# Optimization experiments

Measured on AMD Instinct MI355X. Metric: run time of the kernel, lower is better.

Reference implementation:

```python
import jax, jax.numpy as jnp
import numpy as np

I_SIZE = 4096
H_SIZE = 2048
WIN = 10          # window_size
MAX_DEPTH = 6
EPS = 1e-9


def setup_inputs() -> dict:
    key = jax.random.key(0)
    ks = jax.random.split(key, 10)
    u = lambda k, s: jax.random.uniform(k, s, dtype=jnp.float32)
    n = lambda k, s: jax.random.normal(k, s, dtype=jnp.float32) * 0.02
    return {
        "input": u(ks[0], (WIN, I_SIZE)),
        "stack": u(ks[1], (1, H_SIZE, I_SIZE)),
        "stack_pointer": u(ks[2], (1, H_SIZE)),
        "input_pointer": u(ks[3], (1, WIN + 1)),
        "ff_w": n(ks[4], (I_SIZE, I_SIZE)), "ff_b": jnp.zeros((I_SIZE,), jnp.float32),
        "gate_w": n(ks[5], (2, 1)), "gate_b": jnp.zeros((2,), jnp.float32),
        "kin_w": n(ks[6], (I_SIZE, 2 * I_SIZE)), "kin_b": jnp.zeros((I_SIZE,), jnp.float32),
        "kouth_w": n(ks[7], (I_SIZE, I_SIZE)), "kouth_b": jnp.zeros((I_SIZE,), jnp.float32),
        "kouti_w": n(ks[8], (I_SIZE, I_SIZE)), "kouti_b": jnp.zeros((I_SIZE,), jnp.float32),
    }


def _forward(input, stack, stack_pointer, input_pointer,
             ff_w, ff_b, gate_w, gate_b, kin_w, kin_b,
             kouth_w, kouth_b, kouti_w, kouti_b):
    lsm = jax.nn.log_softmax
    lin = lambda x, w, b: jnp.matmul(x, w.T) + b

    def push(vec, stk, ptr):
        # stk: [1,H,I], ptr: [1,H], vec: [1,I] or [1,1,I]
        stk = stk * (1.0 - ptr)[..., None] + jnp.matmul(ptr[..., None], vec)
        ptr_new = jnp.concatenate([jnp.zeros((ptr.shape[0], 1), ptr.dtype), ptr[:, :-1]], axis=-1)
        return stk, ptr_new

    def pop(stk, ptr):
        ptr_new = jnp.concatenate([ptr[:, 1:], jnp.zeros((ptr.shape[0], 1), ptr.dtype)], axis=-1)
        s = jnp.sum(ptr_new, -1)                      # [1]
        norm = jnp.where(s > 0, ptr_new / jnp.where(s > 0, s, 1.0), ptr_new)
        outvec = jnp.matmul(norm, stk)                # [1,1,I]
        stk_new = (1.0 - ptr_new)[..., None] * stk
        ptr_new = ptr_new.at[:, 0].add(ptr[:, 0])
        return outvec, stk_new, ptr_new

    def get(inp, ptr):
        outvec = jnp.matmul(ptr[:, :-1], inp)         # [1,I]
        ptr_new = jnp.concatenate([jnp.zeros((ptr.shape[0], 1), ptr.dtype), ptr[:, :-1]], axis=-1)
        ptr_new = ptr_new.at[:, -1].add(ptr[:, -1])
        return outvec, ptr_new

    def kld(p, q):
        p = p + EPS
        q = q + EPS
        p = p / jnp.sum(p)
        q = q / jnp.sum(q)
        return jnp.sum(p * jnp.log(p / q))

    def calforward(invec, hvec):
        predvec = lsm(lin(hvec, ff_w, ff_b))
        perp_pred = kld(predvec, invec)
        inp_cat = jnp.concatenate([invec.reshape(1, 1, -1), hvec.reshape(1, 1, -1)], axis=-1)
        new_inp = jnp.exp(lsm(lin(inp_cat, kin_w, kin_b)))      # softmax, [1,1,I]
        proj_hvec = jnp.exp(lsm(lin(new_inp, kouth_w, kouth_b)))
        proj_invec = jnp.exp(lsm(lin(new_inp, kouti_w, kouti_b)))
        perp = perp_pred + kld(proj_invec, invec) / 2 + kld(proj_hvec, hvec) / 2
        gate = jnp.exp(lsm(lin(perp_pred.reshape(1), gate_w, gate_b)))  # [2]
        gate = jnp.where(jnp.sum(hvec) == 0, jnp.array([1.0, 0.0], gate.dtype),
                         jnp.where(jnp.sum(invec) == 0, jnp.array([0.0, 1.0], gate.dtype), gate))
        return gate, perp, new_inp

    stackmem, sptrmem, iptrmem, wldl, perps = [], [], [], [], []
    for ii in range(MAX_DEPTH):
        if ii == 0:
            invec, st1, sp1 = pop(stack, stack_pointer)
            hvec, st1, sp1 = pop(st1, sp1)
            gate, perp, new_inp = calforward(invec, hvec)
            st1, sp1 = push(new_inp, st1, sp1)
            stackmem.append(st1); sptrmem.append(sp1); iptrmem.append(input_pointer)
            wldl.append(gate[1]); perps.append(perp)
        else:
            ip2, st2, sp2 = input_pointer, stack, stack_pointer
            for _ in range(ii - 1):
                invec, ip2 = get(input, ip2)
                st2, sp2 = push(invec, st2, sp2)
            invec, ip2 = get(input, ip2)
            hvec, st2, sp2 = pop(st2, sp2)
            gate, perp, new_inp = calforward(invec, hvec)
            st2, sp2 = push(new_inp, st2, sp2)
            stackmem.append(st2); sptrmem.append(sp2); iptrmem.append(ip2)
            input_avail = 1.0 - ip2[0, -1]
            wldl.append((1.0 - wldl[ii - 1]) * gate[1] * input_avail)
            perps.append(perp)

    w = jnp.stack(wldl)
    w = w / jnp.sum(w)
    resperp = jnp.sum(w * jnp.stack(perps))
    new_stack = sum(w[i] * stackmem[i] for i in range(MAX_DEPTH))
    new_sp = sum(w[i] * sptrmem[i] for i in range(MAX_DEPTH))
    new_ip = sum(w[i] * iptrmem[i] for i in range(MAX_DEPTH))
    ssum = jnp.sum(new_sp, -1, keepdims=True)
    new_sp = jnp.where(ssum > 0, new_sp / jnp.where(ssum > 0, ssum, 1.0), new_sp)
    isum = jnp.sum(new_ip, -1, keepdims=True)
    new_ip = jnp.where(isum > 0, new_ip / jnp.where(isum > 0, isum, 1.0), new_ip)
    return resperp, new_stack, new_sp, new_ip


def reference(input, stack, stack_pointer, input_pointer,
              ff_w, ff_b, gate_w, gate_b, kin_w, kin_b,
              kouth_w, kouth_b, kouti_w, kouti_b):
    return _forward(input, stack, stack_pointer, input_pointer,
                    ff_w, ff_b, gate_w, gate_b, kin_w, kin_b,
                    kouth_w, kouth_b, kouti_w, kouti_b)
```

## Files before the change

kernel.cpp:

```cpp
#include <hip/hip_runtime.h>
#include <cfloat>
#include <cmath>

#define HH   2048
#define ISZ  4096
#define WN   10
#define ND   6
#define EPSF 1e-9f

#define O_WROW   0
#define O_GETW   14336
#define O_POPC   14464
#define O_AVAIL  14496
#define O_SCAL   14528
#define O_IPTR   14592
#define O_DFIN   14720
#define O_CNEW   27008
#define O_CFIN   39296
#define O_SPTR   88448
#define O_NEWINP 100736
#define O_G      125312
#define O_HVEC   145792
#define O_IVEC   170368
#define O_YFF    194944
#define O_Z1     219520
#define O_Z2     244096
#define O_YH     268672
#define O_YI     293248
#define O_RPART  317824

__device__ __forceinline__ float blockReduceSum(float v, float* sm){
  int ln = threadIdx.x & 63, w = threadIdx.x >> 6;
  #pragma unroll
  for (int o=32;o>0;o>>=1) v += __shfl_down(v,o);
  if (ln==0) sm[w]=v;
  __syncthreads();
  if (threadIdx.x==0){
    float r=0.f; int nw=(int)(blockDim.x>>6);
    for (int i=0;i<nw;i++) r+=sm[i];
    sm[16]=r;
  }
  __syncthreads();
  float r = sm[16];
  __syncthreads();
  return r;
}

template<int N>
__device__ __forceinline__ void bRedSumN(float* v, float* sm){
  int ln=threadIdx.x&63, w=threadIdx.x>>6;
  #pragma unroll
  for (int o=32;o>0;o>>=1){
    #pragma unroll
    for (int i=0;i<N;i++) v[i]+=__shfl_down(v[i],o);
  }
  if (ln==0){ for (int i=0;i<N;i++) sm[w*N+i]=v[i]; }
  __syncthreads();
  if (threadIdx.x==0){
    for (int i=0;i<N;i++){ float r=0.f; for (int q=0;q<16;q++) r+=sm[q*N+i]; sm[16*N+i]=r; }
  }
  __syncthreads();
  for (int i=0;i<N;i++) v[i]=sm[16*N+i];
  __syncthreads();
}

template<int N>
__device__ __forceinline__ void bRedMaxN(float* v, float* sm){
  int ln=threadIdx.x&63, w=threadIdx.x>>6;
  #pragma unroll
  for (int o=32;o>0;o>>=1){
    #pragma unroll
    for (int i=0;i<N;i++) v[i]=fmaxf(v[i],__shfl_down(v[i],o));
  }
  if (ln==0){ for (int i=0;i<N;i++) sm[w*N+i]=v[i]; }
  __syncthreads();
  if (threadIdx.x==0){
    for (int i=0;i<N;i++){ float r=-FLT_MAX; for (int q=0;q<16;q++) r=fmaxf(r,sm[q*N+i]); sm[16*N+i]=r; }
  }
  __syncthreads();
  for (int i=0;i<N;i++) v[i]=sm[16*N+i];
  __syncthreads();
}

__global__ __launch_bounds__(1024) void k_ptr_prep(
    const float* __restrict__ sp0g, const float* __restrict__ ip0g,
    float* __restrict__ ws)
{
  __shared__ float sp[HH], q[HH], D[HH];
  __shared__ float c[4][HH];
  __shared__ float red[17];
  const int d   = blockIdx.x;
  const int tid = threadIdx.x;

  float* Wrow = ws + O_WROW;
  float* getW = ws + O_GETW;
  float* popc = ws + O_POPC;
  float* Dfin = ws + O_DFIN;
  float* cnew = ws + O_CNEW;
  float* cfin = ws + O_CFIN;
  float* sptr = ws + O_SPTR;
  float* iptr = ws + O_IPTR;
  float* avail= ws + O_AVAIL;

  if (d==0 && tid==0){
    float ip[WN+1], nip[WN+1];
    for (int k=0;k<=WN;k++) ip[k]=ip0g[k];
    for (int k=0;k<=WN;k++) iptr[k]=ip[k];
    avail[0] = 1.f - ip[WN];
    for (int t=0;t<5;t++){
      for (int k=0;k<WN;k++) getW[t*16+k]=ip[k];
      nip[0]=0.f;
      for (int k=1;k<=WN;k++) nip[k]=ip[k-1];
      nip[WN] += ip[WN];
      for (int k=0;k<=WN;k++) ip[k]=nip[k];
      for (int k=0;k<=WN;k++) iptr[(t+1)*16+k]=ip[k];
      avail[t+1] = 1.f - ip[WN];
    }
  }

  #pragma unroll
  for (int jj=0;jj<2;jj++){ int j=tid+jj*1024; sp[j]=sp0g[j]; D[j]=1.f; }
  __syncthreads();

  if (d==0){
    #pragma unroll
    for (int jj=0;jj<2;jj++){ int j=tid+jj*1024; q[j]=(j<HH-1)? sp[j+1]:0.f; }
    float ls=0.f;
    #pragma unroll
    for (int jj=0;jj<2;jj++) ls += q[tid+jj*1024];
    float s = blockReduceSum(ls, red);
    float sc = (s>0.f)? 1.f/s : 1.f;
    #pragma unroll
    for (int jj=0;jj<2;jj++){
      int j=tid+jj*1024;
      float qq=q[j];
      Wrow[j] = qq*sc;
      D[j] = 1.f - qq;
      sp[j] = qq + ((j==0)? sp[0] : 0.f);
    }
    __syncthreads();
    #pragma unroll
    for (int jj=0;jj<2;jj++){ int j=tid+jj*1024; q[j]=(j<HH-1)? sp[j+1]:0.f; }
    ls=0.f;
    #pragma unroll
    for (int jj=0;jj<2;jj++) ls += q[tid+jj*1024];
    s = blockReduceSum(ls, red);
    sc = (s>0.f)? 1.f/s : 1.f;
    #pragma unroll
    for (int jj=0;jj<2;jj++){
      int j=tid+jj*1024;
      float qq=q[j];
      Wrow[HH+j] = qq*sc*D[j];
      D[j] *= (1.f-qq);
      sp[j] = qq + ((j==0)? sp[0] : 0.f);
    }
    __syncthreads();
    #pragma unroll
    for (int jj=0;jj<2;jj++){
      int j=tid+jj*1024;
      float p=sp[j];
      Dfin[j] = D[j]*(1.f-p);
      cnew[j] = p;
      sptr[j] = (j==0)? 0.f : sp[j-1];
    }
  } else {
    const int nterms = d-1;
    for (int t=0;t<nterms;t++){
      #pragma unroll
      for (int jj=0;jj<2;jj++){
        int j=tid+jj*1024;
        float p=sp[j], f=1.f-p;
        D[j]*=f;
        for (int u=0;u<t;u++) c[u][j]*=f;
        c[t][j]=p;
      }
      __syncthreads();
      float sv[2];
      #pragma unroll
      for (int jj=0;jj<2;jj++){ int j=tid+jj*1024; sv[jj]=(j==0)?0.f:sp[j-1]; }
      __syncthreads();
      #pragma unroll
      for (int jj=0;jj<2;jj++){ int j=tid+jj*1024; sp[j]=sv[jj]; }
      __syncthreads();
    }
    #pragma unroll
    for (int jj=0;jj<2;jj++){ int j=tid+jj*1024; q[j]=(j<HH-1)? sp[j+1]:0.f; }
    float ls=0.f;
    #pragma unroll
    for (int jj=0;jj<2;jj++) ls += q[tid+jj*1024];
    float s = blockReduceSum(ls, red);
    float sc = (s>0.f)? 1.f/s : 1.f;
    for (int t=0;t<nterms;t++){
      float pc=0.f;
      #pragma unroll
      for (int jj=0;jj<2;jj++){ int j=tid+jj*1024; pc += q[j]*sc*c[t][j]; }
      pc = blockReduceSum(pc, red);
      if (tid==0) popc[d*4+t]=pc;
    }
    #pragma unroll
    for (int jj=0;jj<2;jj++){
      int j=tid+jj*1024;
      float qq=q[j];
      Wrow[(1+d)*HH+j] = qq*sc*D[j];
      float f = 1.f-qq;
      D[j] *= f;
      for (int t=0;t<nterms;t++) c[t][j] *= f;
      sp[j] = qq + ((j==0)? sp[0] : 0.f);
    }
    __syncthreads();
    #pragma unroll
    for (int jj=0;jj<2;jj++){
      int j=tid+jj*1024;
      float p=sp[j], f=1.f-p;
      Dfin[d*HH+j] = D[j]*f;
      for (int t=0;t<nterms;t++) cfin[(d*4+t)*HH+j] = c[t][j]*f;
      cnew[d*HH+j] = p;
      sptr[d*HH+j] = (j==0)? 0.f : sp[j-1];
    }
  }
}

__global__ __launch_bounds__(256) void k_rowsum(
    const float* __restrict__ stk, const float* __restrict__ wrow,
    float* __restrict__ Rp)
{
  __shared__ float wsh[7][64];
  const int col = blockIdx.x*256 + threadIdx.x;
  const int by  = blockIdx.y;
  const int r0  = by*64;
  for (int idx=threadIdx.x; idx<7*64; idx+=256){
    int k=idx>>6, r=idx&63;
    wsh[k][r]=wrow[k*HH + r0 + r];
  }
  __syncthreads();
  float a0=0,a1=0,a2=0,a3=0,a4=0,a5=0,a6=0;
  const float* sp = stk + (size_t)r0*ISZ + col;
  #pragma unroll 4
  for (int r=0;r<64;r++){
    float v = sp[(size_t)r*ISZ];
    a0+=wsh[0][r]*v; a1+=wsh[1][r]*v; a2+=wsh[2][r]*v; a3+=wsh[3][r]*v;
    a4+=wsh[4][r]*v; a5+=wsh[5][r]*v; a6+=wsh[6][r]*v;
  }
  Rp[(size_t)(by*7+0)*ISZ+col]=a0; Rp[(size_t)(by*7+1)*ISZ+col]=a1;
  Rp[(size_t)(by*7+2)*ISZ+col]=a2; Rp[(size_t)(by*7+3)*ISZ+col]=a3;
  Rp[(size_t)(by*7+4)*ISZ+col]=a4; Rp[(size_t)(by*7+5)*ISZ+col]=a5;
  Rp[(size_t)(by*7+6)*ISZ+col]=a6;
}

__global__ __launch_bounds__(128) void k_hv(
    const float* __restrict__ input, float* __restrict__ ws)
{
  __shared__ float gwS[80], pcS[24];
  const int tid=threadIdx.x;
  const int cx = blockIdx.x*128 + tid;
  if (tid<80) gwS[tid]=ws[O_GETW+tid];
  if (tid<24) pcS[tid]=ws[O_POPC+tid];
  __syncthreads();
  float inp[WN];
  #pragma unroll
  for (int k=0;k<WN;k++) inp[k]=input[k*ISZ+cx];
  float g[5];
  #pragma unroll
  for (int t=0;t<5;t++){
    float a=0.f;
    #pragma unroll
    for (int k=0;k<WN;k++) a += gwS[t*16+k]*inp[k];
    g[t]=a;
    ws[O_G + t*ISZ + cx]=a;
  }
  float R[7];
  #pragma unroll
  for (int k=0;k<7;k++){
    float a=0.f;
    for (int y=0;y<32;y++) a += ws[O_RPART + (size_t)(y*7+k)*ISZ + cx];
    R[k]=a;
  }
  ws[O_IVEC + cx]=R[0];
  ws[O_HVEC + cx]=R[1];
  #pragma unroll
  for (int d=1;d<ND;d++){
    ws[O_IVEC + d*ISZ + cx] = g[d-1];
    float h = R[1+d];
    for (int t=0;t<=d-2;t++) h += pcS[d*4+t]*g[t];
    ws[O_HVEC + d*ISZ + cx] = h;
  }
}

__device__ __forceinline__ void mv_body2(
    const float* __restrict__ W, int ldw,
    const float* __restrict__ Xg, const float* __restrict__ bias,
    float* __restrict__ Y, int bb)
{
  const int wv = threadIdx.x>>6, ln = threadIdx.x&63;
  const int row0 = bb*16 + wv*2;
  const float* wr0 = W + (size_t)row0*ldw;
  const float* wr1 = wr0 + ldw;
  float a0[6]={0,0,0,0,0,0}, a1[6]={0,0,0,0,0,0};
  #pragma unroll 2
  for (int k=ln*4; k<ISZ; k+=256){
    float4 wa = *(const float4*)(wr0 + k);
    float4 wb = *(const float4*)(wr1 + k);
    #pragma unroll
    for (int d=0; d<6; d++){
      float4 x4 = *(const float4*)(Xg + d*ISZ + k);
      a0[d] += wa.x*x4.x + wa.y*x4.y + wa.z*x4.z + wa.w*x4.w;
      a1[d] += wb.x*x4.x + wb.y*x4.y + wb.z*x4.z + wb.w*x4.w;
    }
  }
  #pragma unroll
  for (int d=0;d<6;d++){
    float v0=a0[d], v1=a1[d];
    #pragma unroll
    for (int o=32;o>0;o>>=1){ v0+=__shfl_down(v0,o); v1+=__shfl_down(v1,o); }
    if (ln==0){
      Y[d*ISZ+row0]   = v0 + (bias? bias[row0]   : 0.f);
      Y[d*ISZ+row0+1] = v1 + (bias? bias[row0+1] : 0.f);
    }
  }
}

__global__ __launch_bounds__(512) void k_matvecA(
    const float* __restrict__ ff_w, const float* __restrict__ ff_b,
    const float* __restrict__ kin_w, const float* __restrict__ kin_b,
    float* __restrict__ ws)
{
  const int task = blockIdx.x >> 8, bb = blockIdx.x & 255;
  if (task==0)      mv_body2(kin_w,     2*ISZ, ws+O_IVEC, kin_b,   ws+O_Z1,  bb);
  else if (task==1) mv_body2(ff_w,      ISZ,   ws+O_HVEC, ff_b,    ws+O_YFF, bb);
  else              mv_body2(kin_w+ISZ, 2*ISZ, ws+O_HVEC, nullptr, ws+O_Z2,  bb);
}

__global__ __launch_bounds__(512) void k_matvecB(
    const float* __restrict__ kouth_w, const float* __restrict__ kouth_b,
    const float* __restrict__ kouti_w, const float* __restrict__ kouti_b,
    float* __restrict__ ws)
{
  const int task = blockIdx.x >> 8, bb = blockIdx.x & 255;
  if (task==0) mv_body2(kouth_w, ISZ, ws+O_NEWINP, kouth_b, ws+O_YH, bb);
  else         mv_body2(kouti_w, ISZ, ws+O_NEWINP, kouti_b, ws+O_YI, bb);
}

__global__ __launch_bounds__(1024) void k_s1(
    const float* __restrict__ gate_w, const float* __restrict__ gate_b,
    float* __restrict__ ws)
{
  __shared__ float sm[96];
  const int d=blockIdx.x, tid=threadIdx.x;
  const float* y  = ws+O_YFF + d*ISZ;
  const float* z1 = ws+O_Z1  + d*ISZ;
  const float* z2 = ws+O_Z2  + d*ISZ;
  const float* iv = ws+O_IVEC+ d*ISZ;
  const float* hv = ws+O_HVEC+ d*ISZ;

  float yv[4], zv[4], ivv[4], hvv[4];
  #pragma unroll
  for (int i=0;i<4;i++){
    int cx=tid+i*1024;
    yv[i]=y[cx]; zv[i]=z1[cx]+z2[cx]; ivv[i]=iv[cx]; hvv[i]=hv[cx];
  }
  float mx[2]={-FLT_MAX,-FLT_MAX};
  #pragma unroll
  for (int i=0;i<4;i++){ mx[0]=fmaxf(mx[0],yv[i]); mx[1]=fmaxf(mx[1],zv[i]); }
  bRedMaxN<2>(mx,sm);

  float s5[5]={0,0,0,0,0};
  #pragma unroll
  for (int i=0;i<4;i++){
    s5[0]+=expf(yv[i]-mx[0]); s5[1]+=expf(zv[i]-mx[1]);
    s5[2]+=yv[i]; s5[3]+=ivv[i]; s5[4]+=hvv[i];
  }
  bRedSumN<5>(s5,sm);
  const float lse = mx[0]+logf(s5[0]);
  const float sP  = s5[2] - (float)ISZ*lse + (float)ISZ*EPSF;
  const float sQ  = s5[3] + (float)ISZ*EPSF;
  const float inv2= 1.f/s5[1];

  float kk[1]={0.f};
  #pragma unroll
  for (int i=0;i<4;i++){
    int cx=tid+i*1024;
    ws[O_NEWINP + d*ISZ + cx] = expf(zv[i]-mx[1])*inv2;
    float ph=((yv[i]-lse)+EPSF)/sP;
    float qh=(ivv[i]+EPSF)/sQ;
    kk[0]+=ph*(logf(ph)-logf(qh));
  }
  bRedSumN<1>(kk,sm);

  if (tid==0){
    float pp=kk[0];
    float a0=gate_w[0]*pp+gate_b[0];
    float a1=gate_w[1]*pp+gate_b[1];
    float mg=fmaxf(a0,a1);
    float e0=expf(a0-mg), e1=expf(a1-mg);
    float g1=e1/(e0+e1);
    if (s5[4]==0.f) g1=0.f;
    else if (s5[3]==0.f) g1=1.f;
    ws[O_SCAL+d]=pp; ws[O_SCAL+6+d]=g1;
    ws[O_SCAL+24+d]=sQ;
    ws[O_SCAL+30+d]=s5[4]+(float)ISZ*EPSF;
  }
}

__global__ __launch_bounds__(1024) void k_s2(float* __restrict__ ws)
{
  __shared__ float sm[96];
  const int d=blockIdx.x, tid=threadIdx.x;
  const float* yh = ws+O_YH  + d*ISZ;
  const float* yi = ws+O_YI  + d*ISZ;
  const float* hv = ws+O_HVEC+ d*ISZ;
  const float* iv = ws+O_IVEC+ d*ISZ;

  float yhv[4], yiv[4], hvv[4], ivv[4];
  #pragma unroll
  for (int i=0;i<4;i++){
    int cx=tid+i*1024;
    yhv[i]=yh[cx]; yiv[i]=yi[cx]; hvv[i]=hv[cx]; ivv[i]=iv[cx];
  }
  float mx[2]={-FLT_MAX,-FLT_MAX};
  #pragma unroll
  for (int i=0;i<4;i++){ mx[0]=fmaxf(mx[0],yhv[i]); mx[1]=fmaxf(mx[1],yiv[i]); }
  bRedMaxN<2>(mx,sm);
  float se[2]={0,0};
  #pragma unroll
  for (int i=0;i<4;i++){ se[0]+=expf(yhv[i]-mx[0]); se[1]+=expf(yiv[i]-mx[1]); }
  bRedSumN<2>(se,sm);
  const float invh=1.f/se[0], invi=1.f/se[1];
  const float spc = 1.f + (float)ISZ*EPSF;
  const float sqh = ws[O_SCAL+30+d], sqi = ws[O_SCAL+24+d];

  float kk[2]={0,0};
  #pragma unroll
  for (int i=0;i<4;i++){
    float ph=(expf(yhv[i]-mx[0])*invh+EPSF)/spc;
    float qh=(hvv[i]+EPSF)/sqh;
    kk[0]+=ph*(logf(ph)-logf(qh));
    float pi=(expf(yiv[i]-mx[1])*invi+EPSF)/spc;
    float qi=(ivv[i]+EPSF)/sqi;
    kk[1]+=pi*(logf(pi)-logf(qi));
  }
  bRedSumN<2>(kk,sm);
  if (tid==0) ws[O_SCAL+12+d] = ws[O_SCAL+d] + 0.5f*(kk[0]+kk[1]);
}

__global__ __launch_bounds__(1024) void k_fin(float* __restrict__ ws,
                                              float* __restrict__ out)
{
  __shared__ float sm[32];
  __shared__ float wsh[ND];
  const int tid=threadIdx.x;
  if (tid==0){
    const float* g1=ws+O_SCAL+6; const float* pp=ws+O_SCAL+12; const float* av=ws+O_AVAIL;
    float wl[ND]; wl[0]=g1[0];
    for (int i=1;i<ND;i++) wl[i]=(1.f-wl[i-1])*g1[i]*av[i];
    float s=0.f; for (int i=0;i<ND;i++) s+=wl[i];
    float rp=0.f;
    for (int i=0;i<ND;i++){ float wn=wl[i]/s; wsh[i]=wn; rp+=wn*pp[i]; }
    out[0]=rp;
  }
  __syncthreads();
  float w[ND];
  #pragma unroll
  for (int dd=0;dd<ND;dd++) w[dd]=wsh[dd];
  const float* sptr=ws+O_SPTR;
  float snl[2], ms=0.f;
  #pragma unroll
  for (int jj=0;jj<2;jj++){
    int j=tid+jj*1024;
    float sn=0.f;
    #pragma unroll
    for (int dd=0;dd<ND;dd++) sn += w[dd]*sptr[dd*HH+j];
    snl[jj]=sn; ms+=sn;
  }
  float t[1]={ms};
  bRedSumN<1>(t,sm);
  float ssum=t[0];
  #pragma unroll
  for (int jj=0;jj<2;jj++){
    int j=tid+jj*1024;
    out[1 + (size_t)HH*ISZ + j] = (ssum>0.f)? snl[jj]/ssum : snl[jj];
  }
  if (tid==0){
    const float* iptr=ws+O_IPTR;
    float ipn[WN+1]; float is=0.f;
    for (int k=0;k<=WN;k++){
      float a=0.f;
      for (int dd=0;dd<ND;dd++) a += w[dd]*iptr[dd*16+k];
      ipn[k]=a; is+=a;
    }
    size_t base = 1 + (size_t)HH*ISZ + HH;
    for (int k=0;k<=WN;k++) out[base+k] = (is>0.f)? ipn[k]/is : ipn[k];
  }
}

__global__ __launch_bounds__(256) void k_stack_out(
    const float* __restrict__ stk, const float* __restrict__ ws,
    float* __restrict__ out)
{
  __shared__ float Vt[10*1024];
  __shared__ float wsh[ND];
  __shared__ float mwS[8];
  __shared__ float ceS[8][10];
  const int tid=threadIdx.x;
  const int c0 = blockIdx.x*1024;
  const int j0 = blockIdx.y*8;

  if (tid==0){
    const float* g1=ws+O_SCAL+6; const float* av=ws+O_AVAIL;
    float wl[ND]; wl[0]=g1[0];
    for (int i=1;i<ND;i++) wl[i]=(1.f-wl[i-1])*g1[i]*av[i];
    float s=0.f; for (int i=0;i<ND;i++) s+=wl[i];
    for (int i=0;i<ND;i++) wsh[i]=wl[i]/s;
  }
  const float* V = ws+O_NEWINP;
  for (int idx=tid; idx<10*1024; idx+=256){
    int v=idx>>10, cc=idx&1023;
    Vt[idx] = V[v*ISZ + c0 + cc];
  }
  __syncthreads();
  if (tid<8){
    int j=j0+tid;
    float mw=0.f, ce[10]={0,0,0,0,0,0,0,0,0,0};
    for (int dd=0;dd<ND;dd++){
      float wd=wsh[dd];
      mw    += wd*ws[O_DFIN+dd*HH+j];
      ce[dd] = wd*ws[O_CNEW+dd*HH+j];
    }
    for (int t=0;t<4;t++){
      float a=0.f;
      for (int dd=t+2;dd<ND;dd++) a += wsh[dd]*ws[O_CFIN+(dd*4+t)*HH+j];
      ce[6+t]=a;
    }
    mwS[tid]=mw;
    for (int v=0;v<10;v++) ceS[tid][v]=ce[v];
  }
  __syncthreads();
  const int tx4 = tid*4;
  for (int r=0;r<8;r++){
    int j=j0+r;
    float mw = mwS[r];
    float4 sv = *(const float4*)(stk + (size_t)j*ISZ + c0 + tx4);
    float o0 = mw*sv.x, o1 = mw*sv.y, o2 = mw*sv.z, o3 = mw*sv.w;
    #pragma unroll
    for (int v=0;v<10;v++){
      const float* vr = Vt + v*1024 + tx4;
      float cv=ceS[r][v];
      o0 += cv*vr[0]; o1 += cv*vr[1]; o2 += cv*vr[2]; o3 += cv*vr[3];
    }
    float* op = out + 1 + (size_t)j*ISZ + c0 + tx4;
    op[0]=o0; op[1]=o1; op[2]=o2; op[3]=o3;
  }
}

extern "C" void kernel_launch(void* const* d_in, const int* in_sizes, int n_in,
                              void* d_out, int out_size, void* d_ws, size_t ws_size,
                              hipStream_t stream)
{
  (void)in_sizes; (void)n_in; (void)out_size; (void)ws_size;
  const float* input   = (const float*)d_in[0];
  const float* stack   = (const float*)d_in[1];
  const float* sp0     = (const float*)d_in[2];
  const float* ip0     = (const float*)d_in[3];
  const float* ff_w    = (const float*)d_in[4];
  const float* ff_b    = (const float*)d_in[5];
  const float* gate_w  = (const float*)d_in[6];
  const float* gate_b  = (const float*)d_in[7];
  const float* kin_w   = (const float*)d_in[8];
  const float* kin_b   = (const float*)d_in[9];
  const float* kouth_w = (const float*)d_in[10];
  const float* kouth_b = (const float*)d_in[11];
  const float* kouti_w = (const float*)d_in[12];
  const float* kouti_b = (const float*)d_in[13];
  float* out = (float*)d_out;
  float* ws  = (float*)d_ws;

  k_ptr_prep<<<ND,1024,0,stream>>>(sp0, ip0, ws);
  k_rowsum<<<dim3(16,32),256,0,stream>>>(stack, ws+O_WROW, ws+O_RPART);
  k_hv<<<32,128,0,stream>>>(input, ws);
  k_matvecA<<<768,512,0,stream>>>(ff_w, ff_b, kin_w, kin_b, ws);
  k_s1<<<ND,1024,0,stream>>>(gate_w, gate_b, ws);
  k_matvecB<<<512,512,0,stream>>>(kouth_w, kouth_b, kouti_w, kouti_b, ws);
  k_s2<<<ND,1024,0,stream>>>(ws);
  k_stack_out<<<dim3(4,256),256,0,stream>>>(stack, ws, out);
  k_fin<<<1,1024,0,stream>>>(ws, out);
}
```

Measured before the change: 204.6 us.

## Split matvec K dimension, stage activations in LDS, prefetch weights into registers

The matvec kernels now split the reduction dimension into two 2048-wide halves, doubling the block count. Each block stages its six activation vectors for that K-chunk in shared memory and issues all of its weight loads up front into registers. The partial results go to new workspace slots and are summed in k_s1 and k_s2. The aim is more parallelism and memory-level concurrency on the weight-bandwidth-bound matvecs. The cost is 48KB of LDS per block, which limits occupancy, plus extra partial-sum traffic.

```diff
diff --git a/kernel.cpp b/kernel.cpp
--- a/kernel.cpp
+++ b/kernel.cpp
@@ -22,12 +22,11 @@
 #define O_G      125312
 #define O_HVEC   145792
 #define O_IVEC   170368
-#define O_YFF    194944
-#define O_Z1     219520
-#define O_Z2     244096
-#define O_YH     268672
-#define O_YI     293248
 #define O_RPART  317824
+#define O_PZ     1235328
+#define O_PYFF   1333632
+#define O_PYH    1382784
+#define O_PYI    1431936
 
 __device__ __forceinline__ float blockReduceSum(float v, float* sm){
   int ln = threadIdx.x & 63, w = threadIdx.x >> 6;
@@ -286,35 +285,52 @@
   }
 }
 
-__device__ __forceinline__ void mv_body2(
-    const float* __restrict__ W, int ldw,
+#define KCH 2048
+
+__device__ __forceinline__ void mv_lds(
+    const float* __restrict__ W, int ldw, int wcol0,
     const float* __restrict__ Xg, const float* __restrict__ bias,
-    float* __restrict__ Y, int bb)
-{
+    float* __restrict__ Yp, int rb, int kbase, float* xls)
+{
+  for (int idx=threadIdx.x; idx<6*KCH/4; idx+=512){
+    int dd = idx>>9, j = idx&511;
+    ((float4*)xls)[idx] = *(const float4*)(Xg + dd*ISZ + kbase + j*4);
+  }
+  __syncthreads();
+
   const int wv = threadIdx.x>>6, ln = threadIdx.x&63;
-  const int row0 = bb*16 + wv*2;
-  const float* wr0 = W + (size_t)row0*ldw;
+  const int row0 = rb*16 + wv*2;
+  const float* wr0 = W + (size_t)row0*ldw + wcol0 + kbase + ln*4;
   const float* wr1 = wr0 + ldw;
+
+  float4 w0[8], w1[8];
+  #pragma unroll
+  for (int i=0;i<8;i++){
+    w0[i] = *(const float4*)(wr0 + i*256);
+    w1[i] = *(const float4*)(wr1 + i*256);
+  }
+
   float a0[6]={0,0,0,0,0,0}, a1[6]={0,0,0,0,0,0};
-  #pragma unroll 2
-  for (int k=ln*4; k<ISZ; k+=256){
-    float4 wa = *(const float4*)(wr0 + k);
-    float4 wb = *(const float4*)(wr1 + k);
-    #pragma unroll
-    for (int d=0; d<6; d++){
-      float4 x4 = *(const float4*)(Xg + d*ISZ + k);
-      a0[d] += wa.x*x4.x + wa.y*x4.y + wa.z*x4.z + wa.w*x4.w;
-      a1[d] += wb.x*x4.x + wb.y*x4.y + wb.z*x4.z + wb.w*x4.w;
-    }
-  }
-  #pragma unroll
-  for (int d=0;d<6;d++){
-    float v0=a0[d], v1=a1[d];
+  #pragma unroll
+  for (int i=0;i<8;i++){
+    float4 x[6];
+    #pragma unroll
+    for (int dd=0;dd<6;dd++) x[dd] = *(const float4*)(xls + dd*KCH + i*256 + ln*4);
+    #pragma unroll
+    for (int dd=0;dd<6;dd++){
+      a0[dd] += w0[i].x*x[dd].x + w0[i].y*x[dd].y + w0[i].z*x[dd].z + w0[i].w*x[dd].w;
+      a1[dd] += w1[i].x*x[dd].x + w1[i].y*x[dd].y + w1[i].z*x[dd].z + w1[i].w*x[dd].w;
+    }
+  }
+
+  #pragma unroll
+  for (int dd=0;dd<6;dd++){
+    float v0=a0[dd], v1=a1[dd];
     #pragma unroll
     for (int o=32;o>0;o>>=1){ v0+=__shfl_down(v0,o); v1+=__shfl_down(v1,o); }
     if (ln==0){
-      Y[d*ISZ+row0]   = v0 + (bias? bias[row0]   : 0.f);
-      Y[d*ISZ+row0+1] = v1 + (bias? bias[row0+1] : 0.f);
+      Yp[dd*ISZ+row0]   = v0 + (bias? bias[row0]   : 0.f);
+      Yp[dd*ISZ+row0+1] = v1 + (bias? bias[row0+1] : 0.f);
     }
   }
 }
@@ -324,10 +340,21 @@
     const float* __restrict__ kin_w, const float* __restrict__ kin_b,
     float* __restrict__ ws)
 {
-  const int task = blockIdx.x >> 8, bb = blockIdx.x & 255;
-  if (task==0)      mv_body2(kin_w,     2*ISZ, ws+O_IVEC, kin_b,   ws+O_Z1,  bb);
-  else if (task==1) mv_body2(ff_w,      ISZ,   ws+O_HVEC, ff_b,    ws+O_YFF, bb);
-  else              mv_body2(kin_w+ISZ, 2*ISZ, ws+O_HVEC, nullptr, ws+O_Z2,  bb);
+  __shared__ float xls[6*KCH];
+  const int task = blockIdx.x >> 9;
+  const int rem  = blockIdx.x & 511;
+  const int ks   = rem >> 8;
+  const int rb   = rem & 255;
+  const int kb   = ks*KCH;
+  if (task==0)
+    mv_lds(kin_w, 2*ISZ, 0,   ws+O_IVEC, (ks==0)?kin_b:nullptr,
+           ws+O_PZ + ks*6*ISZ, rb, kb, xls);
+  else if (task==1)
+    mv_lds(ff_w,  ISZ,   0,   ws+O_HVEC, (ks==0)?ff_b:nullptr,
+           ws+O_PYFF + ks*6*ISZ, rb, kb, xls);
+  else
+    mv_lds(kin_w, 2*ISZ, ISZ, ws+O_HVEC, nullptr,
+           ws+O_PZ + (2+ks)*6*ISZ, rb, kb, xls);
 }
 
 __global__ __launch_bounds__(512) void k_matvecB(
@@ -335,9 +362,18 @@
     const float* __restrict__ kouti_w, const float* __restrict__ kouti_b,
     float* __restrict__ ws)
 {
-  const int task = blockIdx.x >> 8, bb = blockIdx.x & 255;
-  if (task==0) mv_body2(kouth_w, ISZ, ws+O_NEWINP, kouth_b, ws+O_YH, bb);
-  else         mv_body2(kouti_w, ISZ, ws+O_NEWINP, kouti_b, ws+O_YI, bb);
+  __shared__ float xls[6*KCH];
+  const int task = blockIdx.x >> 9;
+  const int rem  = blockIdx.x & 511;
+  const int ks   = rem >> 8;
+  const int rb   = rem & 255;
+  const int kb   = ks*KCH;
+  if (task==0)
+    mv_lds(kouth_w, ISZ, 0, ws+O_NEWINP, (ks==0)?kouth_b:nullptr,
+           ws+O_PYH + ks*6*ISZ, rb, kb, xls);
+  else
+    mv_lds(kouti_w, ISZ, 0, ws+O_NEWINP, (ks==0)?kouti_b:nullptr,
+           ws+O_PYI + ks*6*ISZ, rb, kb, xls);
 }
 
 __global__ __launch_bounds__(1024) void k_s1(
@@ -346,9 +382,6 @@
 {
   __shared__ float sm[96];
   const int d=blockIdx.x, tid=threadIdx.x;
-  const float* y  = ws+O_YFF + d*ISZ;
-  const float* z1 = ws+O_Z1  + d*ISZ;
-  const float* z2 = ws+O_Z2  + d*ISZ;
   const float* iv = ws+O_IVEC+ d*ISZ;
   const float* hv = ws+O_HVEC+ d*ISZ;
 
@@ -356,7 +389,12 @@
   #pragma unroll
   for (int i=0;i<4;i++){
     int cx=tid+i*1024;
-    yv[i]=y[cx]; zv[i]=z1[cx]+z2[cx]; ivv[i]=iv[cx]; hvv[i]=hv[cx];
+    float y=0.f, z=0.f;
+    #pragma unroll
+    for (int s=0;s<2;s++) y += ws[O_PYFF + (s*6+d)*ISZ + cx];
+    #pragma unroll
+    for (int s=0;s<4;s++) z += ws[O_PZ   + (s*6+d)*ISZ + cx];
+    yv[i]=y; zv[i]=z; ivv[i]=iv[cx]; hvv[i]=hv[cx];
   }
   float mx[2]={-FLT_MAX,-FLT_MAX};
   #pragma unroll
@@ -405,8 +443,6 @@
 {
   __shared__ float sm[96];
   const int d=blockIdx.x, tid=threadIdx.x;
-  const float* yh = ws+O_YH  + d*ISZ;
-  const float* yi = ws+O_YI  + d*ISZ;
   const float* hv = ws+O_HVEC+ d*ISZ;
   const float* iv = ws+O_IVEC+ d*ISZ;
 
@@ -414,7 +450,13 @@
   #pragma unroll
   for (int i=0;i<4;i++){
     int cx=tid+i*1024;
-    yhv[i]=yh[cx]; yiv[i]=yi[cx]; hvv[i]=hv[cx]; ivv[i]=iv[cx];
+    float yh=0.f, yi=0.f;
+    #pragma unroll
+    for (int s=0;s<2;s++){
+      yh += ws[O_PYH + (s*6+d)*ISZ + cx];
+      yi += ws[O_PYI + (s*6+d)*ISZ + cx];
+    }
+    yhv[i]=yh; yiv[i]=yi; hvv[i]=hv[cx]; ivv[i]=iv[cx];
   }
   float mx[2]={-FLT_MAX,-FLT_MAX};
   #pragma unroll
@@ -576,9 +618,9 @@
   k_ptr_prep<<<ND,1024,0,stream>>>(sp0, ip0, ws);
   k_rowsum<<<dim3(16,32),256,0,stream>>>(stack, ws+O_WROW, ws+O_RPART);
   k_hv<<<32,128,0,stream>>>(input, ws);
-  k_matvecA<<<768,512,0,stream>>>(ff_w, ff_b, kin_w, kin_b, ws);
+  k_matvecA<<<1536,512,0,stream>>>(ff_w, ff_b, kin_w, kin_b, ws);
   k_s1<<<ND,1024,0,stream>>>(gate_w, gate_b, ws);
-  k_matvecB<<<512,512,0,stream>>>(kouth_w, kouth_b, kouti_w, kouti_b, ws);
+  k_matvecB<<<1024,512,0,stream>>>(kouth_w, kouth_b, kouti_w, kouti_b, ws);
   k_s2<<<ND,1024,0,stream>>>(ws);
   k_stack_out<<<dim3(4,256),256,0,stream>>>(stack, ws, out);
   k_fin<<<1,1024,0,stream>>>(ws, out);
```

New measurement: 216.8 us. +6.0%, slower.
